# Kernel tuning notes

Measured on AMD Instinct MI355X. Metric: run time of the kernel, lower is better.

## Reference

```python
import jax, jax.numpy as jnp
import numpy as np

N_NODES = 100000
N_EDGES = 600000
H = 128


def setup_inputs() -> dict:
    key = jax.random.key(0)
    k_z, k_e, k_w1, k_w2 = jax.random.split(key, 4)
    z = jax.random.normal(k_z, (N_NODES, H), dtype=jnp.float32)
    edge_index = jax.random.randint(k_e, (2, N_EDGES), 0, N_NODES, dtype=jnp.int64)
    # Kaiming-ish init scale for the MLP weights
    W1 = jax.random.normal(k_w1, (2 * H, H), dtype=jnp.float32) * (1.0 / np.sqrt(2 * H))
    b1 = jnp.zeros((H,), dtype=jnp.float32)
    W2 = jax.random.normal(k_w2, (H, 1), dtype=jnp.float32) * (1.0 / np.sqrt(H))
    b2 = jnp.zeros((1,), dtype=jnp.float32)
    return {"z": z, "edge_index": edge_index, "W1": W1, "b1": b1, "W2": W2, "b2": b2}


def reference(z, edge_index, W1, b1, W2, b2):
    # Gather source/destination node embeddings: [E, H] each
    src = z[edge_index[0]]
    dst = z[edge_index[1]]
    # Avoid materializing the [E, 2H] concat: split W1 into src/dst blocks
    # so fc1(cat(src,dst)) == src @ W1[:H] + dst @ W1[H:] + b1
    h = src @ W1[:H] + dst @ W1[H:] + b1  # [E, H]
    h = jax.nn.relu(h)
    out = h @ W2 + b2  # [E, 1]
    return out.reshape(-1)
```

## Files before the change

kernel.cpp:

```cpp
#include <hip/hip_runtime.h>
#include <hip/hip_bf16.h>
#include <stdint.h>

#define N_NODES_C 100000
#define N_EDGES_C 600000
#define H_C 128

typedef __bf16 bf16x8 __attribute__((ext_vector_type(8)));
typedef float f32x16 __attribute__((ext_vector_type(16)));
typedef _Float16 half8 __attribute__((ext_vector_type(8)));
typedef unsigned short ushort8 __attribute__((ext_vector_type(8)));

__device__ __forceinline__ unsigned short f2bf(float f) {
    unsigned int u = __builtin_bit_cast(unsigned int, f);
    u += 0x7fffu + ((u >> 16) & 1u);
    return (unsigned short)(u >> 16);
}

__global__ void w1fmt_kernel(const float* __restrict__ W1,
                             unsigned short* __restrict__ w1f) {
    int i = blockIdx.x * blockDim.x + threadIdx.x;
    if (i >= 8 * 8 * 64 * 8) return;
    int j = i & 7;
    int L = (i >> 3) & 63;
    int t = (i >> 9) & 7;
    int s = (i >> 12) & 7;
    int k  = s * 16 + ((L >> 5) * 8) + j;
    int n2 = t * 32 + (L & 31);
    float w = (n2 < 128) ? W1[k * H_C + n2]
                         : W1[(128 + k) * H_C + (n2 - 128)];
    w1f[i] = f2bf(w);
}

__launch_bounds__(256, 3)
__global__ void node_gemm_kernel(const float* __restrict__ z,
                                 const unsigned short* __restrict__ w1f,
                                 const float* __restrict__ b1,
                                 _Float16* __restrict__ uv) {
    const int lane = threadIdx.x & 63;
    const int wv   = threadIdx.x >> 6;
    const int wid  = blockIdx.x * 4 + wv;
    if (wid >= 2 * (N_NODES_C / 32)) return;
    const int tile = wid >> 1;
    const int uh   = wid & 1;
    const int l31  = lane & 31;
    const int half = lane >> 5;

    const float* arow = z + (size_t)(tile * 32 + l31) * H_C + half * 8;
    f32x16 acc[4] = {};

    #pragma unroll
    for (int s = 0; s < 8; ++s) {
        float4 alo = *reinterpret_cast<const float4*>(arow + s * 16);
        float4 ahi = *reinterpret_cast<const float4*>(arow + s * 16 + 4);
        ushort8 au;
        au[0] = f2bf(alo.x); au[1] = f2bf(alo.y);
        au[2] = f2bf(alo.z); au[3] = f2bf(alo.w);
        au[4] = f2bf(ahi.x); au[5] = f2bf(ahi.y);
        au[6] = f2bf(ahi.z); au[7] = f2bf(ahi.w);
        bf16x8 a = __builtin_bit_cast(bf16x8, au);
        const bf16x8* bp = reinterpret_cast<const bf16x8*>(w1f)
                           + (s * 8 + uh * 4) * 64 + lane;
        #pragma unroll
        for (int t = 0; t < 4; ++t) {
            bf16x8 b = bp[t * 64];
            acc[t] = __builtin_amdgcn_mfma_f32_32x32x16_bf16(a, b, acc[t], 0, 0, 0);
        }
    }

    const int node0 = tile * 32;
    const size_t segbase = uh ? (size_t)N_NODES_C * H_C : 0;
    #pragma unroll
    for (int t = 0; t < 4; ++t) {
        int n = t * 32 + l31;
        float badd = uh ? 0.0f : b1[n];
        #pragma unroll
        for (int r = 0; r < 16; ++r) {
            int row = (r & 3) + 8 * (r >> 2) + 4 * half;
            float v = acc[t][r] + badd;
            float fother = __shfl_xor(v, 1);
            if ((lane & 1) == 0) {
                unsigned int pk = __builtin_bit_cast(
                    unsigned int, __builtin_amdgcn_cvt_pkrtz(v, fother));
                size_t idx = segbase + (size_t)(node0 + row) * H_C + n;
                *reinterpret_cast<unsigned int*>(uv + idx) = pk;
            }
        }
    }
}

__global__ void edge_kernel(const _Float16* __restrict__ uv,
                            const int* __restrict__ ei,
                            const float* __restrict__ w2,
                            const float* __restrict__ b2,
                            float* __restrict__ out) {
    const int tid = blockIdx.x * blockDim.x + threadIdx.x;
    const int j   = tid & 15;
    const int q   = tid >> 4;
    const int e0  = q * 4;
    if (e0 >= N_EDGES_C) return;

    float w2v[8];
    {
        float4 a = *reinterpret_cast<const float4*>(w2 + j * 8);
        float4 b = *reinterpret_cast<const float4*>(w2 + j * 8 + 4);
        w2v[0] = a.x; w2v[1] = a.y; w2v[2] = a.z; w2v[3] = a.w;
        w2v[4] = b.x; w2v[5] = b.y; w2v[6] = b.z; w2v[7] = b.w;
    }
    const float c2 = b2[0];
    const _Float16* vbase = uv + (size_t)N_NODES_C * H_C;

    int4 ss = *reinterpret_cast<const int4*>(ei + e0);
    int4 dd = *reinterpret_cast<const int4*>(ei + N_EDGES_C + e0);

    half8 u0 = *reinterpret_cast<const half8*>(uv    + (size_t)ss.x * H_C + j * 8);
    half8 v0 = *reinterpret_cast<const half8*>(vbase + (size_t)dd.x * H_C + j * 8);
    half8 u1 = *reinterpret_cast<const half8*>(uv    + (size_t)ss.y * H_C + j * 8);
    half8 v1 = *reinterpret_cast<const half8*>(vbase + (size_t)dd.y * H_C + j * 8);
    half8 u2 = *reinterpret_cast<const half8*>(uv    + (size_t)ss.z * H_C + j * 8);
    half8 v2 = *reinterpret_cast<const half8*>(vbase + (size_t)dd.z * H_C + j * 8);
    half8 u3 = *reinterpret_cast<const half8*>(uv    + (size_t)ss.w * H_C + j * 8);
    half8 v3 = *reinterpret_cast<const half8*>(vbase + (size_t)dd.w * H_C + j * 8);

    float p0 = 0.0f, p1 = 0.0f, p2 = 0.0f, p3 = 0.0f;
    #pragma unroll
    for (int k = 0; k < 8; ++k) {
        float h0 = (float)u0[k] + (float)v0[k];
        float h1 = (float)u1[k] + (float)v1[k];
        float h2 = (float)u2[k] + (float)v2[k];
        float h3 = (float)u3[k] + (float)v3[k];
        h0 = h0 > 0.0f ? h0 : 0.0f;
        h1 = h1 > 0.0f ? h1 : 0.0f;
        h2 = h2 > 0.0f ? h2 : 0.0f;
        h3 = h3 > 0.0f ? h3 : 0.0f;
        p0 = fmaf(h0, w2v[k], p0);
        p1 = fmaf(h1, w2v[k], p1);
        p2 = fmaf(h2, w2v[k], p2);
        p3 = fmaf(h3, w2v[k], p3);
    }
    #pragma unroll
    for (int m = 1; m <= 8; m <<= 1) {
        p0 += __shfl_xor(p0, m);
        p1 += __shfl_xor(p1, m);
        p2 += __shfl_xor(p2, m);
        p3 += __shfl_xor(p3, m);
    }
    if (j == 0) {
        float4 o = { p0 + c2, p1 + c2, p2 + c2, p3 + c2 };
        *reinterpret_cast<float4*>(out + e0) = o;
    }
}

extern "C" void kernel_launch(void* const* d_in, const int* in_sizes, int n_in,
                              void* d_out, int out_size, void* d_ws, size_t ws_size,
                              hipStream_t stream) {
    const float* z  = (const float*)d_in[0];
    const int*   ei = (const int*)d_in[1];
    const float* W1 = (const float*)d_in[2];
    const float* b1 = (const float*)d_in[3];
    const float* W2 = (const float*)d_in[4];
    const float* b2 = (const float*)d_in[5];
    float* out = (float*)d_out;

    unsigned short* w1f = (unsigned short*)d_ws;
    _Float16* uv = (_Float16*)((char*)d_ws + 65536);

    w1fmt_kernel<<<(8 * 8 * 64 * 8 + 255) / 256, 256, 0, stream>>>(W1, w1f);

    int nwaves = 2 * (N_NODES_C / 32);
    node_gemm_kernel<<<(nwaves + 3) / 4, 256, 0, stream>>>(z, w1f, b1, uv);

    int nquarters = N_EDGES_C / 4;
    edge_kernel<<<(nquarters * 16 + 255) / 256, 256, 0, stream>>>(uv, ei, W2, b2, out);
}
```

Before: 162.4 us.

## Make node GEMM persistent with register-resident W1 fragments per wave

The node GEMM becomes a persistent grid-stride kernel over 32-node tiles. Each of the four waves in a block loads its two column-slices of the formatted W1 into registers once and reuses them for every tile. All eight A-fragment loads are issued up front before the MFMAs, which helps hide latency. This removes repeated W1 loads from global or L2 and lets all four waves share the same z tile, but it costs more registers (launch bounds drop to 2 blocks) and caps the grid at 1024 blocks.

Result: no change. 164.3 us (+1.2%).

```diff
diff --git a/kernel.cpp b/kernel.cpp
--- a/kernel.cpp
+++ b/kernel.cpp
@@ -32,58 +32,74 @@
     w1f[i] = f2bf(w);
 }
 
-__launch_bounds__(256, 3)
+__launch_bounds__(256, 2)
 __global__ void node_gemm_kernel(const float* __restrict__ z,
                                  const unsigned short* __restrict__ w1f,
                                  const float* __restrict__ b1,
                                  _Float16* __restrict__ uv) {
     const int lane = threadIdx.x & 63;
     const int wv   = threadIdx.x >> 6;
-    const int wid  = blockIdx.x * 4 + wv;
-    if (wid >= 2 * (N_NODES_C / 32)) return;
-    const int tile = wid >> 1;
-    const int uh   = wid & 1;
     const int l31  = lane & 31;
     const int half = lane >> 5;
+    const int uh   = wv >> 1;
 
-    const float* arow = z + (size_t)(tile * 32 + l31) * H_C + half * 8;
-    f32x16 acc[4] = {};
-
+    bf16x8 bfrag[8][2];
     #pragma unroll
     for (int s = 0; s < 8; ++s) {
-        float4 alo = *reinterpret_cast<const float4*>(arow + s * 16);
-        float4 ahi = *reinterpret_cast<const float4*>(arow + s * 16 + 4);
-        ushort8 au;
-        au[0] = f2bf(alo.x); au[1] = f2bf(alo.y);
-        au[2] = f2bf(alo.z); au[3] = f2bf(alo.w);
-        au[4] = f2bf(ahi.x); au[5] = f2bf(ahi.y);
-        au[6] = f2bf(ahi.z); au[7] = f2bf(ahi.w);
-        bf16x8 a = __builtin_bit_cast(bf16x8, au);
-        const bf16x8* bp = reinterpret_cast<const bf16x8*>(w1f)
-                           + (s * 8 + uh * 4) * 64 + lane;
         #pragma unroll
-        for (int t = 0; t < 4; ++t) {
-            bf16x8 b = bp[t * 64];
-            acc[t] = __builtin_amdgcn_mfma_f32_32x32x16_bf16(a, b, acc[t], 0, 0, 0);
+        for (int t = 0; t < 2; ++t) {
+            bfrag[s][t] = reinterpret_cast<const bf16x8*>(w1f)
+                              [(s * 8 + wv * 2 + t) * 64 + lane];
         }
     }
 
-    const int node0 = tile * 32;
+    float badd[2];
+    int   ncol[2];
+    #pragma unroll
+    for (int t = 0; t < 2; ++t) {
+        int n2  = (wv * 2 + t) * 32 + l31;
+        ncol[t] = n2 - uh * 128;
+        badd[t] = uh ? 0.0f : b1[n2];
+    }
     const size_t segbase = uh ? (size_t)N_NODES_C * H_C : 0;
-    #pragma unroll
-    for (int t = 0; t < 4; ++t) {
-        int n = t * 32 + l31;
-        float badd = uh ? 0.0f : b1[n];
+
+    for (int tile = blockIdx.x; tile < N_NODES_C / 32; tile += gridDim.x) {
+        const float* arow = z + (size_t)(tile * 32 + l31) * H_C + half * 8;
+
+        float4 alo[8], ahi[8];
         #pragma unroll
-        for (int r = 0; r < 16; ++r) {
-            int row = (r & 3) + 8 * (r >> 2) + 4 * half;
-            float v = acc[t][r] + badd;
-            float fother = __shfl_xor(v, 1);
-            if ((lane & 1) == 0) {
-                unsigned int pk = __builtin_bit_cast(
-                    unsigned int, __builtin_amdgcn_cvt_pkrtz(v, fother));
-                size_t idx = segbase + (size_t)(node0 + row) * H_C + n;
-                *reinterpret_cast<unsigned int*>(uv + idx) = pk;
+        for (int s = 0; s < 8; ++s) {
+            alo[s] = *reinterpret_cast<const float4*>(arow + s * 16);
+            ahi[s] = *reinterpret_cast<const float4*>(arow + s * 16 + 4);
+        }
+
+        f32x16 acc[2] = {};
+        #pragma unroll
+        for (int s = 0; s < 8; ++s) {
+            ushort8 au;
+            au[0] = f2bf(alo[s].x); au[1] = f2bf(alo[s].y);
+            au[2] = f2bf(alo[s].z); au[3] = f2bf(alo[s].w);
+            au[4] = f2bf(ahi[s].x); au[5] = f2bf(ahi[s].y);
+            au[6] = f2bf(ahi[s].z); au[7] = f2bf(ahi[s].w);
+            bf16x8 a = __builtin_bit_cast(bf16x8, au);
+            acc[0] = __builtin_amdgcn_mfma_f32_32x32x16_bf16(a, bfrag[s][0], acc[0], 0, 0, 0);
+            acc[1] = __builtin_amdgcn_mfma_f32_32x32x16_bf16(a, bfrag[s][1], acc[1], 0, 0, 0);
+        }
+
+        const int node0 = tile * 32;
+        #pragma unroll
+        for (int t = 0; t < 2; ++t) {
+            #pragma unroll
+            for (int r = 0; r < 16; ++r) {
+                int row = (r & 3) + 8 * (r >> 2) + 4 * half;
+                float v = acc[t][r] + badd[t];
+                float fo = __shfl_xor(v, 1);
+                if ((lane & 1) == 0) {
+                    unsigned int pk = __builtin_bit_cast(
+                        unsigned int, __builtin_amdgcn_cvt_pkrtz(v, fo));
+                    size_t idx = segbase + (size_t)(node0 + row) * H_C + ncol[t];
+                    *reinterpret_cast<unsigned int*>(uv + idx) = pk;
+                }
             }
         }
     }
@@ -167,8 +183,7 @@
 
     w1fmt_kernel<<<(8 * 8 * 64 * 8 + 255) / 256, 256, 0, stream>>>(W1, w1f);
 
-    int nwaves = 2 * (N_NODES_C / 32);
-    node_gemm_kernel<<<(nwaves + 3) / 4, 256, 0, stream>>>(z, w1f, b1, uv);
+    node_gemm_kernel<<<1024, 256, 0, stream>>>(z, w1f, b1, uv);
 
     int nquarters = N_EDGES_C / 4;
     edge_kernel<<<(nquarters * 16 + 255) / 256, 256, 0, stream>>>(uv, ei, W2, b2, out);
```
